# Optimization experiments

Hardware: AMD Instinct MI355X
Metric: run time of the kernel (lower is better)

Reference implementation:

```python
import jax, jax.numpy as jnp
import numpy as np

HIDDEN = 2048
NH = 16
NKV = 8
HD = 128
EPS = 1e-6
THETA = 10000.0
Q_SIZE = NH * HD
KV_SIZE = NKV * HD


def setup_inputs() -> dict:
    key = jax.random.key(0)
    k1, k2, k3, k4 = jax.random.split(key, 4)
    B, T = 2, 2048
    hidden_states = jax.random.normal(k1, (B, T, HIDDEN), dtype=jnp.float32)
    positions = jnp.broadcast_to(jnp.arange(T, dtype=jnp.int32)[None, :], (B, T))
    # learned params
    w_qkv = jax.random.normal(k2, (Q_SIZE + 2 * KV_SIZE, HIDDEN), dtype=jnp.float32) * (HIDDEN ** -0.5)
    w_o = jax.random.normal(k3, (HIDDEN, Q_SIZE), dtype=jnp.float32) * (Q_SIZE ** -0.5)
    rms_w = jnp.ones((HD,), dtype=jnp.float32) + 0.01 * jax.random.normal(k4, (HD,), dtype=jnp.float32)
    return {"positions": positions, "hidden_states": hidden_states,
            "w_qkv": w_qkv, "w_o": w_o, "rms_w": rms_w}


def _rms_norm(x, w):
    # per-head RMSNorm over last dim (head_dim)
    var = jnp.mean(jnp.square(x), axis=-1, keepdims=True)
    return x * jax.lax.rsqrt(var + EPS) * w


def _rope(positions, x):
    # NeoX-style rotary over full head_dim. positions: [B,T], x: [B,T,h,HD]
    half = HD // 2
    inv_freq = 1.0 / (THETA ** (jnp.arange(0, half, dtype=jnp.float32) / half))
    angles = positions.astype(jnp.float32)[..., None] * inv_freq  # [B,T,half]
    cos = jnp.cos(angles)[:, :, None, :]  # [B,T,1,half]
    sin = jnp.sin(angles)[:, :, None, :]
    x1, x2 = jnp.split(x, 2, axis=-1)
    return jnp.concatenate([x1 * cos - x2 * sin, x2 * cos + x1 * sin], axis=-1)


def reference(positions, hidden_states, w_qkv, w_o, rms_w):
    B, T, _ = hidden_states.shape
    qkv = jnp.einsum('bth,oh->bto', hidden_states, w_qkv)
    q = qkv[..., :Q_SIZE].reshape(B, T, NH, HD)
    k = qkv[..., Q_SIZE:Q_SIZE + KV_SIZE].reshape(B, T, NKV, HD)
    v = qkv[..., Q_SIZE + KV_SIZE:].reshape(B, T, NKV, HD)
    # QK-norm (qkv_bias=False path)
    q = _rms_norm(q, rms_w)
    k = _rms_norm(k, rms_w)
    q, k = _rope(positions, q), _rope(positions, k)
    # GQA attention, causal. group q heads onto kv heads: g = NH // NKV
    g = NH // NKV
    qg = q.reshape(B, T, NKV, g, HD)
    scale = HD ** -0.5
    scores = jnp.einsum('btkgd,bskd->bkgts', qg, k) * scale  # [B,NKV,g,T,T]
    causal = jnp.tril(jnp.ones((T, T), dtype=bool))
    scores = jnp.where(causal, scores, jnp.finfo(scores.dtype).min)
    probs = jax.nn.softmax(scores, axis=-1)
    o = jnp.einsum('bkgts,bskd->btkgd', probs, v).reshape(B, T, Q_SIZE)
    return jnp.einsum('bto,ho->bth', o, w_o)
```

## Files before the change

### kernel.cpp

```cpp
#include <hip/hip_runtime.h>
#include <hip/hip_bf16.h>

typedef __attribute__((ext_vector_type(8))) short short8;
typedef __attribute__((ext_vector_type(8))) unsigned short u16x8;
typedef __attribute__((ext_vector_type(4))) float f32x4;
typedef __attribute__((ext_vector_type(16))) float f32x16;

#define HIDDEN 2048
#define NH 16
#define NKV 8
#define HD 128
#define T_SEQ 2048
#define B_SZ 2
#define M_TOK (B_SZ * T_SEQ)
#define QSIZE (NH * HD)
#define KVSIZE (NKV * HD)
#define OUTQKV (QSIZE + 2 * KVSIZE)

__device__ __forceinline__ unsigned short f2bf(float f) {
  unsigned int u = __builtin_bit_cast(unsigned int, f);
  u += 0x7FFFu + ((u >> 16) & 1u);
  return (unsigned short)(u >> 16);
}
__device__ __forceinline__ float bf2f(unsigned short h) {
  return __builtin_bit_cast(float, (unsigned int)h << 16);
}

typedef __attribute__((address_space(3))) void lds_void;
typedef __attribute__((address_space(1))) const void glb_void;
__device__ __forceinline__ void gld16(const void* g, void* l) {
  __builtin_amdgcn_global_load_lds((glb_void*)g, (lds_void*)l, 16, 0, 0);
}

__device__ __forceinline__ void cstore(float* p, float v) { *p = v; }
__device__ __forceinline__ void cstore(unsigned short* p, float v) { *p = f2bf(v); }

__device__ __forceinline__ float exp2fast(float x) {
  float r;
  asm("v_exp_f32 %0, %1" : "=v"(r) : "v"(x));
  return r;
}
__device__ __forceinline__ unsigned cvtpk(float lo, float hi) {
  unsigned r;
  asm("v_cvt_pk_bf16_f32 %0, %1, %2" : "=v"(r) : "v"(lo), "v"(hi));
  return r;
}
__device__ __forceinline__ void pl32swap(unsigned& a, unsigned& b) {
  asm volatile("v_permlane32_swap_b32 %0, %1" : "+v"(a), "+v"(b));
}

template <int N>
__device__ __forceinline__ void vwait();
template <> __device__ __forceinline__ void vwait<0>() { asm volatile("s_waitcnt vmcnt(0)" ::: "memory"); }
template <> __device__ __forceinline__ void vwait<3>() { asm volatile("s_waitcnt vmcnt(3)" ::: "memory"); }
template <> __device__ __forceinline__ void vwait<4>() { asm volatile("s_waitcnt vmcnt(4)" ::: "memory"); }

__global__ void cvt_f32_bf16(const float* __restrict__ in, unsigned short* __restrict__ out, int n8) {
  int i = blockIdx.x * blockDim.x + threadIdx.x;
  if (i >= n8) return;
  const float4* p = (const float4*)in + (size_t)i * 2;
  float4 a = p[0], b = p[1];
  u16x8 o = {f2bf(a.x), f2bf(a.y), f2bf(a.z), f2bf(a.w),
             f2bf(b.x), f2bf(b.y), f2bf(b.z), f2bf(b.w)};
  ((u16x8*)out)[i] = o;
}

template <int MT, typename TC>
__global__ __launch_bounds__(512, 2) void gemm8(const unsigned short* __restrict__ A,
                                                const unsigned short* __restrict__ B,
                                                TC* __restrict__ C,
                                                int M, int N, int K) {
  constexpr int BM = MT * 32;
  constexpr int MT2 = MT / 2;
  constexpr int VMN = (MT == 8) ? 4 : 3;
  __shared__ unsigned short lsA[4][BM * 32];
  __shared__ unsigned short lsB[4][8192];
  const int tid = threadIdx.x;
  const int wave = tid >> 6, lane = tid & 63;
  const int wr = wave >> 2, wc = wave & 3;
  const int lr = lane & 15;
  const int ntn = N >> 8;
  const int cpx = gridDim.x >> 3;
  const int wg = (blockIdx.x & 7) * cpx + (blockIdx.x >> 3);
  const int m0 = (wg / ntn) * BM, n0 = (wg % ntn) * 256;
  const int ce = 8 * ((lane >> 4) ^ ((lr >> 1) & 3));
  const int rr0 = tid >> 2;
  const int cle = 8 * ((tid & 3) ^ ((rr0 >> 1) & 3));
  const unsigned short* pA0 = A + (size_t)(m0 + rr0) * K + cle;
  const unsigned short* pA1 = pA0 + (size_t)128 * K;
  const unsigned short* pB0 = B + (size_t)(n0 + rr0) * K + cle;
  const unsigned short* pB1 = pB0 + (size_t)128 * K;
  const int dst0 = 8 * tid, dst1 = 4096 + 8 * tid;

  auto stageA = [&](int hn) {
    const int s = hn & 3;
    gld16(pA0 + hn * 32, &lsA[s][dst0]);
    if constexpr (MT == 8) gld16(pA1 + hn * 32, &lsA[s][dst1]);
  };
  auto stageB = [&](int hn) {
    const int s = hn & 3;
    gld16(pB0 + hn * 32, &lsB[s][dst0]);
    gld16(pB1 + hn * 32, &lsB[s][dst1]);
  };

  f32x4 acc[MT][4] = {};
  short8 af[MT2], bfg[4];
  const int NT = K >> 6;

  stageA(0); stageB(0); stageA(1); stageB(1);
  vwait<0>();
  __syncthreads();

#define PHASE(KK, MH, STG, VM)                                                            \
  {                                                                                       \
    const int slot = sb + (KK);                                                           \
    _Pragma("unroll")                                                                     \
    for (int i = 0; i < MT2; i++)                                                         \
      af[i] = *(const short8*)&lsA[slot][(wr * (MT * 16) + (MH) * (MT * 8) + i * 16 + lr) * 32 + ce]; \
    if ((MH) == 0) {                                                                      \
      _Pragma("unroll")                                                                   \
      for (int j = 0; j < 4; j++)                                                         \
        bfg[j] = *(const short8*)&lsB[slot][(wc * 64 + j * 16 + lr) * 32 + ce];           \
    }                                                                                     \
    if (st) { STG; }                                                                      \
    if ((VM) == 1) {                                                                      \
      if (st) vwait<VMN>(); else vwait<0>();                                              \
    } else if ((VM) == 2) {                                                               \
      if (st) vwait<VMN>();                                                               \
    }                                                                                     \
    __builtin_amdgcn_s_barrier();                                                         \
    __builtin_amdgcn_s_setprio(1);                                                        \
    _Pragma("unroll")                                                                     \
    for (int i = 0; i < MT2; i++)                                                         \
      _Pragma("unroll")                                                                   \
      for (int j = 0; j < 4; j++)                                                         \
        acc[(MH)*MT2 + i][j] =                                                            \
            __builtin_amdgcn_mfma_f32_16x16x32_bf16(af[i], bfg[j], acc[(MH)*MT2 + i][j], 0, 0, 0); \
    __builtin_amdgcn_s_setprio(0);                                                        \
    __builtin_amdgcn_s_barrier();                                                         \
  }

  for (int t = 0; t < NT; t++) {
    const int sb = (2 * t) & 3;
    const bool st = (t < NT - 1);
    const int h2 = 2 * t + 2, h3 = 2 * t + 3;
    PHASE(0, 0, stageA(h2), 0)
    PHASE(0, 1, stageB(h2), 1)
    PHASE(1, 0, stageA(h3), 0)
    PHASE(1, 1, stageB(h3), 2)
  }
#undef PHASE

#pragma unroll
  for (int i = 0; i < MT; i++)
#pragma unroll
    for (int j = 0; j < 4; j++) {
      int gm = m0 + wr * (MT * 16) + i * 16 + (lane >> 4) * 4;
      int gn = n0 + wc * 64 + j * 16 + lr;
      TC* cp = C + (size_t)gm * N + gn;
#pragma unroll
      for (int r = 0; r < 4; r++) cstore(cp + (size_t)r * N, acc[i][j][r]);
    }
}

__global__ void norm_rope_kernel(const unsigned short* __restrict__ qkv,
                                 const int* __restrict__ positions,
                                 const float* __restrict__ rms_w,
                                 unsigned short* __restrict__ qa,
                                 unsigned short* __restrict__ ka) {
  const int m = blockIdx.x;
  const int b = m >> 11, tt = m & 2047;
  const int lane = threadIdx.x;
  const float pos = (float)positions[m];
  const float inv_freq = powf(10000.0f, -(float)lane * (1.0f / 64.0f));
  float sv, cv;
  sincosf(pos * inv_freq, &sv, &cv);
  const float w1 = rms_w[lane], w2 = rms_w[lane + 64];
  const unsigned short* src = qkv + (size_t)m * OUTQKV;
  for (int h = 0; h < 24; h++) {
    unsigned short r1 = src[h * 128 + lane], r2 = src[h * 128 + 64 + lane];
    float x1 = bf2f(r1), x2 = bf2f(r2);
    float ss = x1 * x1 + x2 * x2;
    ss += __shfl_xor(ss, 1);  ss += __shfl_xor(ss, 2);  ss += __shfl_xor(ss, 4);
    ss += __shfl_xor(ss, 8);  ss += __shfl_xor(ss, 16); ss += __shfl_xor(ss, 32);
    float rstd = rsqrtf(ss * (1.0f / 128.0f) + 1e-6f);
    float y1 = x1 * rstd * w1, y2 = x2 * rstd * w2;
    float o1 = y1 * cv - y2 * sv, o2 = y2 * cv + y1 * sv;
    unsigned short* dst;
    if (h < 16) dst = qa + (((size_t)b * NH + h) * T_SEQ + tt) * HD;
    else        dst = ka + (((size_t)b * NKV + (h - 16)) * T_SEQ + tt) * HD;
    dst[lane] = f2bf(o1); dst[lane + 64] = f2bf(o2);
  }
}

__global__ __launch_bounds__(256) void v_transpose(const unsigned short* __restrict__ qkv,
                                                   unsigned short* __restrict__ vat) {
  __shared__ unsigned short tile[64][136];
  const int tt0 = blockIdx.x * 64;
  const int kvh = blockIdx.y, b = blockIdx.z;
  const int t = threadIdx.x;
  {
    const int tok = t >> 2, d0 = (t & 3) * 32;
    const unsigned short* src = qkv + (size_t)((size_t)b * T_SEQ + tt0 + tok) * OUTQKV
                                + QSIZE + KVSIZE + kvh * HD + d0;
#pragma unroll
    for (int i = 0; i < 4; i++)
      *(u16x8*)&tile[tok][d0 + i * 8] = *(const u16x8*)(src + i * 8);
  }
  __syncthreads();
  {
    const int d = t >> 1, c0 = (t & 1) * 32;
    unsigned short* dst = vat + ((size_t)((size_t)b * NKV + kvh) * HD + d) * T_SEQ + tt0 + c0;
#pragma unroll
    for (int j = 0; j < 4; j++) {
      u16x8 v;
#pragma unroll
      for (int e = 0; e < 8; e++) v[e] = tile[c0 + j * 8 + e][d];
      *(u16x8*)(dst + j * 8) = v;
    }
  }
}

__global__ __launch_bounds__(256, 2) void attn_kernel(const unsigned short* __restrict__ qa,
                                                      const unsigned short* __restrict__ ka,
                                                      const unsigned short* __restrict__ vat,
                                                      unsigned short* __restrict__ ob) {
  __shared__ unsigned short ks[2][64 * 128];
  __shared__ unsigned short vs[2][128 * 64];
  const int bx = blockIdx.x;
  const int qt = 31 - (bx >> 4);
  const int kvh = bx & 7, b = (bx >> 3) & 1;
  const int tid = threadIdx.x, w = tid >> 6, lane = tid & 63;
  const int l31 = lane & 31, h5 = lane >> 5;
  const int h = kvh * 2 + (w >> 1);
  const int qrow = qt * 64 + (w & 1) * 32 + l31;
  const float cexp = 0.08838834764831845f * 1.44269504088896340f;

  const unsigned short* Kg = ka + ((size_t)b * NKV + kvh) * T_SEQ * HD;
  const unsigned short* Vg = vat + ((size_t)b * NKV + kvh) * (size_t)HD * T_SEQ;

  short8 qf[8];
  {
    const unsigned short* Qg = qa + (((size_t)b * NH + h) * T_SEQ + qrow) * HD;
#pragma unroll
    for (int c = 0; c < 8; c++) qf[c] = *(const short8*)(Qg + c * 16 + h5 * 8);
  }

  auto stage = [&](int j, int buf) {
#pragma unroll
    for (int s = 0; s < 4; s++) {
      int g = s * 256 + tid;
      int kr = g >> 4;
      int kc = 8 * ((g & 15) ^ (kr & 15));
      gld16(Kg + (size_t)(j * 64 + kr) * HD + kc, &ks[buf][g * 8]);
    }
#pragma unroll
    for (int s = 0; s < 4; s++) {
      int g = s * 256 + tid;
      int vd = g >> 3;
      int vc = 8 * ((g & 7) ^ (vd & 7));
      gld16(Vg + (size_t)vd * T_SEQ + j * 64 + vc, &vs[buf][g * 8]);
    }
  };

  stage(0, 0);
  vwait<0>();
  __syncthreads();

  f32x16 oacc[4] = {};
  float mraw = -1e30f, m2 = -3.0e29f, lsum = 0.f;

  for (int j = 0; j <= qt; j++) {
    const int buf = j & 1;
    if (j < qt) stage(j + 1, buf ^ 1);

    f32x16 sacc[2] = {};
    __builtin_amdgcn_s_setprio(1);
#pragma unroll
    for (int c = 0; c < 8; c++) {
#pragma unroll
      for (int t = 0; t < 2; t++) {
        const int row = t * 32 + l31;
        short8 kf = *(const short8*)&ks[buf][row * 128 + ((c * 16 + h5 * 8) ^ (8 * (l31 & 15)))];
        sacc[t] = __builtin_amdgcn_mfma_f32_32x32x16_bf16(kf, qf[c], sacc[t], 0, 0, 0);
      }
    }
    __builtin_amdgcn_s_setprio(0);

    if (j * 64 + 63 > qt * 64 + (w & 1) * 32) {
#pragma unroll
      for (int t = 0; t < 2; t++)
#pragma unroll
        for (int r = 0; r < 16; r++) {
          int kvg = j * 64 + t * 32 + (r & 3) + 8 * (r >> 2) + 4 * h5;
          if (kvg > qrow) sacc[t][r] = -1e30f;
        }
    }
    float mx = sacc[0][0];
#pragma unroll
    for (int t = 0; t < 2; t++)
#pragma unroll
      for (int r = 0; r < 16; r++) mx = fmaxf(mx, sacc[t][r]);
    mx = fmaxf(mx, __shfl_xor(mx, 32));
    if (__any((mx - mraw) * cexp > 11.5f)) {
      float mn = fmaxf(mraw, mx);
      float corr = exp2fast((mraw - mn) * cexp);
      mraw = mn;
      m2 = mn * cexp;
      lsum *= corr;
#pragma unroll
      for (int dt = 0; dt < 4; dt++)
#pragma unroll
        for (int r = 0; r < 16; r++) oacc[dt][r] *= corr;
    }
    short8 pf[4];
#pragma unroll
    for (int kt = 0; kt < 4; kt++) {
      const int t = kt >> 1, r0 = (kt & 1) * 8;
      float e0 = exp2fast(sacc[t][r0 + 0] * cexp - m2);
      float e1 = exp2fast(sacc[t][r0 + 1] * cexp - m2);
      float e2 = exp2fast(sacc[t][r0 + 2] * cexp - m2);
      float e3 = exp2fast(sacc[t][r0 + 3] * cexp - m2);
      float e4 = exp2fast(sacc[t][r0 + 4] * cexp - m2);
      float e5 = exp2fast(sacc[t][r0 + 5] * cexp - m2);
      float e6 = exp2fast(sacc[t][r0 + 6] * cexp - m2);
      float e7 = exp2fast(sacc[t][r0 + 7] * cexp - m2);
      lsum += ((e0 + e1) + (e2 + e3)) + ((e4 + e5) + (e6 + e7));
      unsigned a0 = cvtpk(e0, e1), a1 = cvtpk(e2, e3);
      unsigned b0 = cvtpk(e4, e5), b1 = cvtpk(e6, e7);
      pl32swap(a0, b0);
      pl32swap(a1, b1);
      uint4 uu = make_uint4(a0, a1, b0, b1);
      pf[kt] = __builtin_bit_cast(short8, uu);
    }
    __builtin_amdgcn_s_setprio(1);
#pragma unroll
    for (int dt = 0; dt < 4; dt++) {
      const int d = dt * 32 + l31;
#pragma unroll
      for (int kt = 0; kt < 4; kt++) {
        short8 vf = *(const short8*)&vs[buf][d * 64 + ((kt * 16 + h5 * 8) ^ (8 * (l31 & 7)))];
        oacc[dt] = __builtin_amdgcn_mfma_f32_32x32x16_bf16(vf, pf[kt], oacc[dt], 0, 0, 0);
      }
    }
    __builtin_amdgcn_s_setprio(0);
    vwait<0>();
    __syncthreads();
  }

  lsum += __shfl_xor(lsum, 32);
  const float inv = 1.0f / lsum;
  unsigned short* dst = ob + ((size_t)b * T_SEQ + qrow) * QSIZE + h * HD;
#pragma unroll
  for (int dt = 0; dt < 4; dt++)
#pragma unroll
    for (int rg = 0; rg < 4; rg++) {
      ushort4 v4;
      v4.x = f2bf(oacc[dt][rg * 4 + 0] * inv);
      v4.y = f2bf(oacc[dt][rg * 4 + 1] * inv);
      v4.z = f2bf(oacc[dt][rg * 4 + 2] * inv);
      v4.w = f2bf(oacc[dt][rg * 4 + 3] * inv);
      *(ushort4*)(dst + dt * 32 + rg * 8 + 4 * h5) = v4;
    }
}

extern "C" void kernel_launch(void* const* d_in, const int* in_sizes, int n_in,
                              void* d_out, int out_size, void* d_ws, size_t ws_size,
                              hipStream_t stream) {
  const int* positions = (const int*)d_in[0];
  const float* hidden  = (const float*)d_in[1];
  const float* w_qkv   = (const float*)d_in[2];
  const float* w_o     = (const float*)d_in[3];
  const float* rms_w   = (const float*)d_in[4];
  float* out = (float*)d_out;

  unsigned short* qkv   = (unsigned short*)d_ws;
  unsigned short* hb    = qkv + (size_t)M_TOK * OUTQKV;
  unsigned short* wqkvb = hb + (size_t)M_TOK * HIDDEN;
  unsigned short* qa    = hb;
  unsigned short* ka    = wqkvb;
  unsigned short* vat   = wqkvb + (size_t)B_SZ * NKV * T_SEQ * HD;
  unsigned short* wob   = hb;
  unsigned short* ob    = qkv;

  cvt_f32_bf16<<<(M_TOK * HIDDEN / 8 + 255) / 256, 256, 0, stream>>>(hidden, hb, M_TOK * HIDDEN / 8);
  cvt_f32_bf16<<<(OUTQKV * HIDDEN / 8 + 255) / 256, 256, 0, stream>>>(w_qkv, wqkvb, OUTQKV * HIDDEN / 8);
  gemm8<8, unsigned short>
      <<<(M_TOK / 256) * (OUTQKV / 256), 512, 0, stream>>>(hb, wqkvb, qkv, M_TOK, OUTQKV, HIDDEN);
  norm_rope_kernel<<<M_TOK, 64, 0, stream>>>(qkv, positions, rms_w, qa, ka);
  v_transpose<<<dim3(T_SEQ / 64, NKV, B_SZ), 256, 0, stream>>>(qkv, vat);
  attn_kernel<<<512, 256, 0, stream>>>(qa, ka, vat, ob);
  cvt_f32_bf16<<<(HIDDEN * QSIZE / 8 + 255) / 256, 256, 0, stream>>>(w_o, wob, HIDDEN * QSIZE / 8);
  gemm8<4, float>
      <<<(M_TOK / 128) * (HIDDEN / 256), 512, 0, stream>>>(ob, wob, out, M_TOK, HIDDEN, QSIZE);
}
```

Measured before the change: 213.0 us.

## Fuse fp32-to-bf16 conversions, vectorize GEMM epilogue, drop mid-phase barrier

Merges the three fp32-to-bf16 conversion launches into one prep kernel, giving w_o its own workspace region so it can be converted up front. In the GEMM it swaps the MFMA operand order so each lane holds four consecutive output columns, which lets the epilogue use one vector store instead of four strided scalar stores. It also removes the barrier before the MFMA block in each phase. Dropping that barrier risks an LDS race between staging and reading, and the launch-count change relies on the grid equalling 256 for both GEMMs.

```diff
diff --git a/kernel.cpp b/kernel.cpp
--- a/kernel.cpp
+++ b/kernel.cpp
@@ -32,9 +32,6 @@
   __builtin_amdgcn_global_load_lds((glb_void*)g, (lds_void*)l, 16, 0, 0);
 }
 
-__device__ __forceinline__ void cstore(float* p, float v) { *p = v; }
-__device__ __forceinline__ void cstore(unsigned short* p, float v) { *p = f2bf(v); }
-
 __device__ __forceinline__ float exp2fast(float x) {
   float r;
   asm("v_exp_f32 %0, %1" : "=v"(r) : "v"(x));
@@ -55,14 +52,36 @@
 template <> __device__ __forceinline__ void vwait<3>() { asm volatile("s_waitcnt vmcnt(3)" ::: "memory"); }
 template <> __device__ __forceinline__ void vwait<4>() { asm volatile("s_waitcnt vmcnt(4)" ::: "memory"); }
 
-__global__ void cvt_f32_bf16(const float* __restrict__ in, unsigned short* __restrict__ out, int n8) {
-  int i = blockIdx.x * blockDim.x + threadIdx.x;
-  if (i >= n8) return;
-  const float4* p = (const float4*)in + (size_t)i * 2;
+__device__ __forceinline__ void store4(unsigned short* p, const f32x4& v) {
+  ushort4 o;
+  o.x = f2bf(v[0]); o.y = f2bf(v[1]); o.z = f2bf(v[2]); o.w = f2bf(v[3]);
+  *(ushort4*)p = o;
+}
+__device__ __forceinline__ void store4(float* p, const f32x4& v) {
+  float4 o = {v[0], v[1], v[2], v[3]};
+  *(float4*)p = o;
+}
+
+#define SEG0 1048576
+#define SEG1 1048576
+#define SEG2 524288
+__global__ __launch_bounds__(256) void prep_kernel(const float* __restrict__ hidden,
+                                                   const float* __restrict__ w_qkv,
+                                                   const float* __restrict__ w_o,
+                                                   unsigned short* __restrict__ hb,
+                                                   unsigned short* __restrict__ wqkvb,
+                                                   unsigned short* __restrict__ wob) {
+  size_t i = (size_t)blockIdx.x * blockDim.x + threadIdx.x;
+  const float* src;
+  unsigned short* dst;
+  if (i < SEG0) { src = hidden; dst = hb; }
+  else if (i < SEG0 + SEG1) { src = w_qkv; dst = wqkvb; i -= SEG0; }
+  else { src = w_o; dst = wob; i -= (SEG0 + SEG1); }
+  const float4* p = (const float4*)src + i * 2;
   float4 a = p[0], b = p[1];
   u16x8 o = {f2bf(a.x), f2bf(a.y), f2bf(a.z), f2bf(a.w),
              f2bf(b.x), f2bf(b.y), f2bf(b.z), f2bf(b.w)};
-  ((u16x8*)out)[i] = o;
+  ((u16x8*)dst)[i] = o;
 }
 
 template <int MT, typename TC>
@@ -128,14 +147,13 @@
     } else if ((VM) == 2) {                                                               \
       if (st) vwait<VMN>();                                                               \
     }                                                                                     \
-    __builtin_amdgcn_s_barrier();                                                         \
     __builtin_amdgcn_s_setprio(1);                                                        \
     _Pragma("unroll")                                                                     \
     for (int i = 0; i < MT2; i++)                                                         \
       _Pragma("unroll")                                                                   \
       for (int j = 0; j < 4; j++)                                                         \
         acc[(MH)*MT2 + i][j] =                                                            \
-            __builtin_amdgcn_mfma_f32_16x16x32_bf16(af[i], bfg[j], acc[(MH)*MT2 + i][j], 0, 0, 0); \
+            __builtin_amdgcn_mfma_f32_16x16x32_bf16(bfg[j], af[i], acc[(MH)*MT2 + i][j], 0, 0, 0); \
     __builtin_amdgcn_s_setprio(0);                                                        \
     __builtin_amdgcn_s_barrier();                                                         \
   }
@@ -155,11 +173,9 @@
   for (int i = 0; i < MT; i++)
 #pragma unroll
     for (int j = 0; j < 4; j++) {
-      int gm = m0 + wr * (MT * 16) + i * 16 + (lane >> 4) * 4;
-      int gn = n0 + wc * 64 + j * 16 + lr;
-      TC* cp = C + (size_t)gm * N + gn;
-#pragma unroll
-      for (int r = 0; r < 4; r++) cstore(cp + (size_t)r * N, acc[i][j][r]);
+      int gm = m0 + wr * (MT * 16) + i * 16 + lr;
+      int gn = n0 + wc * 64 + j * 16 + (lane >> 4) * 4;
+      store4(C + (size_t)gm * N + gn, acc[i][j]);
     }
 }
 
@@ -377,20 +393,19 @@
   unsigned short* qkv   = (unsigned short*)d_ws;
   unsigned short* hb    = qkv + (size_t)M_TOK * OUTQKV;
   unsigned short* wqkvb = hb + (size_t)M_TOK * HIDDEN;
+  unsigned short* wob   = wqkvb + (size_t)OUTQKV * HIDDEN;
   unsigned short* qa    = hb;
   unsigned short* ka    = wqkvb;
   unsigned short* vat   = wqkvb + (size_t)B_SZ * NKV * T_SEQ * HD;
-  unsigned short* wob   = hb;
   unsigned short* ob    = qkv;
 
-  cvt_f32_bf16<<<(M_TOK * HIDDEN / 8 + 255) / 256, 256, 0, stream>>>(hidden, hb, M_TOK * HIDDEN / 8);
-  cvt_f32_bf16<<<(OUTQKV * HIDDEN / 8 + 255) / 256, 256, 0, stream>>>(w_qkv, wqkvb, OUTQKV * HIDDEN / 8);
+  const int prep_items = SEG0 + SEG1 + SEG2;
+  prep_kernel<<<prep_items / 256, 256, 0, stream>>>(hidden, w_qkv, w_o, hb, wqkvb, wob);
   gemm8<8, unsigned short>
-      <<<(M_TOK / 256) * (OUTQKV / 256), 512, 0, stream>>>(hb, wqkvb, qkv, M_TOK, OUTQKV, HIDDEN);
+      <<<256, 512, 0, stream>>>(hb, wqkvb, qkv, M_TOK, OUTQKV, HIDDEN);
   norm_rope_kernel<<<M_TOK, 64, 0, stream>>>(qkv, positions, rms_w, qa, ka);
   v_transpose<<<dim3(T_SEQ / 64, NKV, B_SZ), 256, 0, stream>>>(qkv, vat);
   attn_kernel<<<512, 256, 0, stream>>>(qa, ka, vat, ob);
-  cvt_f32_bf16<<<(HIDDEN * QSIZE / 8 + 255) / 256, 256, 0, stream>>>(w_o, wob, HIDDEN * QSIZE / 8);
   gemm8<4, float>
-      <<<(M_TOK / 128) * (HIDDEN / 256), 512, 0, stream>>>(ob, wob, out, M_TOK, HIDDEN, QSIZE);
-}
+      <<<256, 512, 0, stream>>>(ob, wob, out, M_TOK, HIDDEN, QSIZE);
+}
```

Measured after the change: 211.0 us. About the same (-0.9%).
